# Optimization experiments

Hardware: AMD Instinct MI355X
Metric: run time of the kernel (lower is better)

The kernel has to match this reference:

```python
import jax, jax.numpy as jnp
import numpy as np

B, T, D = 8, 1024, 1024
KD, VD, H = 1024, 1024, 16  # key_dim_total, value_dim_total, num_heads
NEG = -1e9
EPS = 1e-5


def setup_inputs() -> dict:
    key = jax.random.key(0)
    ks = jax.random.split(key, 8)
    x = jax.random.normal(ks[0], (B, T, D), dtype=jnp.float32)
    x_lens = jax.random.randint(ks[1], (B,), 1, T + 1).astype(jnp.int32)
    ln_gamma = jnp.ones((D,), jnp.float32)
    ln_beta = jnp.zeros((D,), jnp.float32)
    qkv_out = 2 * KD + VD
    w_qkv = jax.random.normal(ks[2], (D, qkv_out), jnp.float32) / np.sqrt(D)
    b_qkv = jax.random.normal(ks[3], (qkv_out,), jnp.float32) * 0.01
    w_out = jax.random.normal(ks[4], (VD, D), jnp.float32) / np.sqrt(VD)
    b_out = jax.random.normal(ks[5], (D,), jnp.float32) * 0.01
    return {"x": x, "x_lens": x_lens, "ln_gamma": ln_gamma, "ln_beta": ln_beta,
            "w_qkv": w_qkv, "b_qkv": b_qkv, "w_out": w_out, "b_out": b_out}


def reference(x, x_lens, ln_gamma, ln_beta, w_qkv, b_qkv, w_out, b_out):
    # LayerNorm over feature dim
    mu = jnp.mean(x, axis=-1, keepdims=True)
    var = jnp.mean(jnp.square(x - mu), axis=-1, keepdims=True)
    xn = (x - mu) * jax.lax.rsqrt(var + EPS) * ln_gamma + ln_beta
    # fused QKV projection
    qkv = xn @ w_qkv + b_qkv  # (B, T, 2*KD+VD)
    q, k, v = qkv[..., :KD], qkv[..., KD:2 * KD], qkv[..., 2 * KD:]
    hd = KD // H
    q = q.reshape(B, T, H, hd).transpose(0, 2, 1, 3)  # (B,H,T,hd)
    k = k.reshape(B, T, H, hd).transpose(0, 2, 1, 3)
    v = v.reshape(B, T, H, VD // H).transpose(0, 2, 1, 3)
    scale = 1.0 / np.sqrt(hd)
    scores = jnp.einsum("bhtd,bhsd->bhts", q, k) * scale  # (B,H,T,T)
    # combined causal + kv-length padding mask (additive in original; boolean here)
    causal = jnp.tril(jnp.ones((T, T), bool))  # (T,T)
    kv_valid = jnp.arange(T)[None, :] < x_lens[:, None]  # (B,T)
    mask = causal[None, None, :, :] & kv_valid[:, None, None, :]
    scores = jnp.where(mask, scores, NEG)
    att = jax.nn.softmax(scores, axis=-1)
    att_out = jnp.einsum("bhts,bhsd->bhtd", att, v)  # (B,H,T,hd_v)
    out = att_out.transpose(0, 2, 1, 3).reshape(B, T, VD)
    out = out @ w_out + b_out
    return out
```

## Files before the change

kernel.cpp:

```cpp
#include <hip/hip_runtime.h>

#define D_MODEL 1024
#define T_SEQ   1024
#define BATCH   8
#define NHEAD   16
#define HDIM    64

typedef float      v4f   __attribute__((ext_vector_type(4)));
typedef _Float16   half8 __attribute__((ext_vector_type(8)));
typedef _Float16   half4h __attribute__((ext_vector_type(4)));
typedef unsigned int ui4 __attribute__((ext_vector_type(4)));

__device__ __forceinline__ void load_lds16(const _Float16* g, _Float16* l) {
  __builtin_amdgcn_global_load_lds(
      (const __attribute__((address_space(1))) unsigned int*)g,
      (__attribute__((address_space(3))) unsigned int*)l, 16, 0, 0);
}

__global__ __launch_bounds__(256) void ln_kernel(const float* __restrict__ x,
                                                 const float* __restrict__ gamma,
                                                 const float* __restrict__ beta,
                                                 _Float16* __restrict__ xn) {
  int row = blockIdx.x;
  int tid = threadIdx.x;
  const float* xr = x + (size_t)row * D_MODEL;
  v4f xv = *(const v4f*)(xr + tid * 4);
  float s  = xv[0] + xv[1] + xv[2] + xv[3];
  float sq = xv[0]*xv[0] + xv[1]*xv[1] + xv[2]*xv[2] + xv[3]*xv[3];
#pragma unroll
  for (int off = 32; off > 0; off >>= 1) {
    s  += __shfl_xor(s, off);
    sq += __shfl_xor(sq, off);
  }
  __shared__ float ps[4], psq[4];
  int wave = tid >> 6;
  if ((tid & 63) == 0) { ps[wave] = s; psq[wave] = sq; }
  __syncthreads();
  float tot  = ps[0] + ps[1] + ps[2] + ps[3];
  float totq = psq[0] + psq[1] + psq[2] + psq[3];
  float mean = tot * (1.0f / D_MODEL);
  float var  = totq * (1.0f / D_MODEL) - mean * mean;
  float rs   = rsqrtf(var + 1e-5f);
  v4f gv = *(const v4f*)(gamma + tid * 4);
  v4f bv = *(const v4f*)(beta + tid * 4);
  half4h o;
#pragma unroll
  for (int i = 0; i < 4; ++i)
    o[i] = (_Float16)((xv[i] - mean) * rs * gv[i] + bv[i]);
  *(half4h*)(xn + (size_t)row * D_MODEL + tid * 4) = o;
}

__global__ __launch_bounds__(256) void fragize_kernel(const float* __restrict__ W,
                                                      _Float16* __restrict__ Bf,
                                                      int N, int K) {
  int g = blockIdx.x * 256 + threadIdx.x;
  int lane = g & 63, tile = g >> 6;
  int ktiles = K >> 5;
  int kt = tile % ktiles, nt = tile / ktiles;
  int n  = nt * 16 + (lane & 15);
  int k0 = kt * 32 + (lane >> 4) * 8;
  half8 o;
#pragma unroll
  for (int j = 0; j < 8; ++j) o[j] = (_Float16)W[(size_t)(k0 + j) * N + n];
  *(half8*)(Bf + (size_t)g * 8) = o;
}

__global__ __launch_bounds__(256) void wtrans_kernel(const float* __restrict__ W,
                                                     _Float16* __restrict__ Wt,
                                                     int N, int K) {
  __shared__ _Float16 t[64][72];
  int k0 = blockIdx.x * 64, n0 = blockIdx.y * 64;
  int tid = threadIdx.x;
  int r = tid >> 3, c = (tid & 7) * 8;
#pragma unroll
  for (int it = 0; it < 2; ++it) {
    int row = r + it * 32;
    const float* src = W + (size_t)(k0 + row) * N + n0 + c;
    v4f x0 = *(const v4f*)src;
    v4f x1 = *(const v4f*)(src + 4);
#pragma unroll
    for (int j = 0; j < 4; ++j) t[row][c + j] = (_Float16)x0[j];
#pragma unroll
    for (int j = 0; j < 4; ++j) t[row][c + 4 + j] = (_Float16)x1[j];
  }
  __syncthreads();
#pragma unroll
  for (int it = 0; it < 2; ++it) {
    int d = r + it * 32;
    half8 o;
#pragma unroll
    for (int j = 0; j < 8; ++j) o[j] = t[c + j][d];
    *(half8*)(Wt + (size_t)(n0 + d) * K + k0 + c) = o;
  }
}

__global__ __launch_bounds__(256) void vtrans_kernel(const _Float16* __restrict__ Vd,
                                                     _Float16* __restrict__ Vt) {
  __shared__ _Float16 tile[64][68];
  int p  = blockIdx.y;
  int t0 = blockIdx.x * 64;
  int tid = threadIdx.x;
  int r = tid >> 3, c = (tid & 7) * 8;
#pragma unroll
  for (int it = 0; it < 2; ++it) {
    int rr = r + it * 32;
    *(ui4*)&tile[rr][c] = *(const ui4*)&Vd[((size_t)p * T_SEQ + t0 + rr) * HDIM + c];
  }
  __syncthreads();
#pragma unroll
  for (int it = 0; it < 2; ++it) {
    int d = r + it * 32;
    half8 o;
#pragma unroll
    for (int j = 0; j < 8; ++j) o[j] = tile[c + j][d];
    *(half8*)&Vt[((size_t)p * HDIM + d) * T_SEQ + t0 + c] = o;
  }
}


#define BAR   __builtin_amdgcn_s_barrier()
#define LGKM0 asm volatile("s_waitcnt lgkmcnt(0)" ::: "memory")
#define VMC2  asm volatile("s_waitcnt vmcnt(2)" ::: "memory")
#define PRIO1 __builtin_amdgcn_s_setprio(1)
#define PRIO0 __builtin_amdgcn_s_setprio(0)

#define RDA(dst, BUF, KK)                                                       \
  _Pragma("unroll")                                                             \
  for (int d2 = 0; d2 < 4; ++d2)                                                \
    dst[d2] = *(const half8*)(lds + (BUF) +                                     \
                              (wm + d2 * 16 + l15) * 64 +                       \
                              ((((KK) * 4 + quad) ^ swz) * 8));

#define RDB(dst, BUF, NI0, KK)                                                  \
  _Pragma("unroll")                                                             \
  for (int n2 = 0; n2 < 2; ++n2)                                                \
    dst[n2] = *(const half8*)(lds + (BUF) + 8192 +                              \
                              (wn + ((NI0) + n2) * 16 + l15) * 64 +             \
                              ((((KK) * 4 + quad) ^ swz) * 8));

#define MFQ(A_, B_, NI0)                                                        \
  _Pragma("unroll")                                                             \
  for (int mi = 0; mi < 4; ++mi)                                                \
    _Pragma("unroll")                                                           \
    for (int n2 = 0; n2 < 2; ++n2)                                              \
      acc[mi][(NI0) + n2] = __builtin_amdgcn_mfma_f32_16x16x32_f16(             \
          A_[mi], B_[n2], acc[mi][(NI0) + n2], 0, 0, 0);

#define STGA(BUF, R0, KT)                                                       \
  load_lds16(Asrc + (size_t)(R0) * 1024 + (KT) * 64, ldst + (BUF) + (R0) * 64)
#define STGB(BUF, R0, KT)                                                       \
  load_lds16(Bsrc + (size_t)(R0) * 1024 + (KT) * 64, ldst + (BUF) + 8192 + (R0) * 64)

__global__ __launch_bounds__(512, 2) void gemm256_qkv(
    const _Float16* __restrict__ A, const _Float16* __restrict__ Bt,
    const float* __restrict__ bias,
    _Float16* __restrict__ Qd, _Float16* __restrict__ Kd, _Float16* __restrict__ Vd) {
  __shared__ _Float16 lds[49152];
  const int K = 1024;
  int tid  = threadIdx.x;
  int wave = tid >> 6, lane = tid & 63;
  int l15  = lane & 15, quad = lane >> 4;
  int wm = (wave & 1) * 64, wn = (wave >> 1) * 64;
  int m0 = blockIdx.x * 128, n0 = blockIdx.y * 256;
  int swz = l15 & 7;

  int ric = tid >> 3;
  int colofs = ((tid & 7) ^ (ric & 7)) * 8;
  const _Float16* Asrc = A  + (size_t)(m0 + ric) * K + colofs;
  const _Float16* Bsrc = Bt + (size_t)(n0 + ric) * K + colofs;
  _Float16* ldst = lds + wave * 512;

  const int B0 = 0, B1 = 24576;
  v4f acc[4][4];
  v4f zero = {0.f, 0.f, 0.f, 0.f};
#pragma unroll
  for (int i = 0; i < 4; ++i)
#pragma unroll
    for (int j = 0; j < 4; ++j) acc[i][j] = zero;

  STGA(B0, 0, 0); STGA(B0, 64, 0);
  STGB(B0, 0, 0); STGB(B0, 64, 0); STGB(B0, 128, 0); STGB(B0, 192, 0);
  STGA(B1, 0, 1); STGA(B1, 64, 1);
  VMC2; BAR;

  half8 a0[4], a1[4], bl[2], bh[2];
#pragma unroll 1
  for (int i = 0; i < 8; ++i) {
    int kt1 = 2 * i + 1;
    int kt2 = (2 * i + 2 < 16) ? 2 * i + 2 : 15;
    int kt3 = (2 * i + 3 < 16) ? 2 * i + 3 : 15;
    RDA(a0, B0, 0); RDB(bl, B0, 0, 0);
    STGB(B1, 0, kt1); STGB(B1, 64, kt1);
    BAR; LGKM0; PRIO1; MFQ(a0, bl, 0); PRIO0; BAR;
    RDB(bh, B0, 2, 0);
    STGB(B1, 128, kt1); STGB(B1, 192, kt1);
    BAR; LGKM0; PRIO1; MFQ(a0, bh, 2); PRIO0; BAR;
    RDA(a1, B0, 1); RDB(bl, B0, 0, 1);
    BAR; LGKM0; PRIO1; MFQ(a1, bl, 0); PRIO0; BAR;
    RDB(bh, B0, 2, 1);
    STGA(B0, 0, kt2); STGA(B0, 64, kt2);
    VMC2; BAR; LGKM0; PRIO1; MFQ(a1, bh, 2); PRIO0; BAR;
    RDA(a0, B1, 0); RDB(bl, B1, 0, 0);
    STGB(B0, 0, kt2); STGB(B0, 64, kt2);
    BAR; LGKM0; PRIO1; MFQ(a0, bl, 0); PRIO0; BAR;
    RDB(bh, B1, 2, 0);
    STGB(B0, 128, kt2); STGB(B0, 192, kt2);
    BAR; LGKM0; PRIO1; MFQ(a0, bh, 2); PRIO0; BAR;
    RDA(a1, B1, 1); RDB(bl, B1, 0, 1);
    BAR; LGKM0; PRIO1; MFQ(a1, bl, 0); PRIO0; BAR;
    RDB(bh, B1, 2, 1);
    STGA(B1, 0, kt3); STGA(B1, 64, kt3);
    VMC2; BAR; LGKM0; PRIO1; MFQ(a1, bh, 2); PRIO0; BAR;
  }

  float bv[4];
#pragma unroll
  for (int ni = 0; ni < 4; ++ni) bv[ni] = bias[n0 + wn + ni * 16 + l15];
  int sec = n0 >> 10;
  _Float16* dstP = sec == 0 ? Qd : (sec == 1 ? Kd : Vd);
  float scale = sec == 0 ? 0.18033688f : 1.0f;
#pragma unroll
  for (int mi = 0; mi < 4; ++mi)
#pragma unroll
    for (int ni = 0; ni < 4; ++ni) {
      int n = n0 + wn + ni * 16 + l15;
      int h = (n >> 6) & 15, d = n & 63;
#pragma unroll
      for (int r = 0; r < 4; ++r) {
        int m = m0 + wm + mi * 16 + quad * 4 + r;
        int b = m >> 10, t = m & 1023;
        float v = acc[mi][ni][r] + bv[ni];
        dstP[((size_t)(b * NHEAD + h) * T_SEQ + t) * HDIM + d] = (_Float16)(v * scale);
      }
    }
}

template <int MODE>
__global__ __launch_bounds__(256) void gemm_kernel(
    const _Float16* __restrict__ A, const _Float16* __restrict__ Bfrag,
    const float* __restrict__ bias, int M, int N, int K,
    float* __restrict__ outF,
    _Float16* __restrict__ Qd, _Float16* __restrict__ Kd, _Float16* __restrict__ Vd) {
  __shared__ _Float16 As[2][128 * 32];
  int tid = threadIdx.x;
  int wave = tid >> 6, lane = tid & 63;
  int l15 = lane & 15, quad = lane >> 4;
  int wm = (wave & 1) * 64, wn = (wave >> 1) * 64;
  int m0 = blockIdx.x * 128, n0 = blockIdx.y * 128;
  v4f zero = {0.f, 0.f, 0.f, 0.f};
  v4f acc[4][4];
#pragma unroll
  for (int i = 0; i < 4; ++i)
#pragma unroll
    for (int j = 0; j < 4; ++j) acc[i][j] = zero;

  int ar0 = tid >> 2;
  int akc = (tid & 3) * 8;
  const _Float16* Ap = A + (size_t)(m0 + ar0) * K + akc;
  _Float16* AsW0 = &As[0][0] + wave * 512;
  _Float16* AsW1 = &As[1][0] + wave * 512;
  const int ktiles = K >> 5;
  const _Float16* Bp = Bfrag + (size_t)((n0 + wn) >> 4) * ktiles * 512 + lane * 8;

  load_lds16(Ap, AsW0);
  load_lds16(Ap + (size_t)64 * K, AsW0 + 2048);
  for (int kt = 0; kt < ktiles; ++kt) {
    int cur = kt & 1;
    __syncthreads();
    if (kt + 1 < ktiles) {
      _Float16* nx = cur ? AsW0 : AsW1;
      load_lds16(Ap + (kt + 1) * 32,                  nx);
      load_lds16(Ap + (kt + 1) * 32 + (size_t)64 * K, nx + 2048);
    }
    half8 bf[4];
#pragma unroll
    for (int ni = 0; ni < 4; ++ni)
      bf[ni] = *(const half8*)(Bp + ((size_t)ni * ktiles + kt) * 512);
    half8 af[4];
#pragma unroll
    for (int i = 0; i < 4; ++i)
      af[i] = *(const half8*)&As[cur][(wm + i * 16 + l15) * 32 + quad * 8];
#pragma unroll
    for (int mi = 0; mi < 4; ++mi)
#pragma unroll
      for (int ni = 0; ni < 4; ++ni)
        acc[mi][ni] = __builtin_amdgcn_mfma_f32_16x16x32_f16(af[mi], bf[ni], acc[mi][ni], 0, 0, 0);
  }
  float bv[4];
#pragma unroll
  for (int ni = 0; ni < 4; ++ni) bv[ni] = bias[n0 + wn + ni * 16 + l15];
#pragma unroll
  for (int mi = 0; mi < 4; ++mi) {
#pragma unroll
    for (int ni = 0; ni < 4; ++ni) {
      int n = n0 + wn + ni * 16 + l15;
#pragma unroll
      for (int r = 0; r < 4; ++r) {
        int m = m0 + wm + mi * 16 + quad * 4 + r;
        float v = acc[mi][ni][r] + bv[ni];
        if (MODE == 1) {
          outF[(size_t)m * N + n] = v;
        } else {
          int b = m >> 10, t = m & 1023;
          int h = (n >> 6) & 15, d = n & 63;
          size_t idx = ((size_t)(b * NHEAD + h) * T_SEQ + t) * HDIM + d;
          if (n < 1024)        Qd[idx] = (_Float16)(v * 0.18033688f);
          else if (n < 2048)   Kd[idx] = (_Float16)v;
          else                 Vd[idx] = (_Float16)v;
        }
      }
    }
  }
}

__global__ __launch_bounds__(256) void attn_kernel(const _Float16* __restrict__ Qg,
                                                   const _Float16* __restrict__ Kk,
                                                   const _Float16* __restrict__ Vt,
                                                   const int* __restrict__ x_lens,
                                                   _Float16* __restrict__ att) {
  __shared__ _Float16 Ks[2][64 * 32];
  __shared__ _Float16 Vs[2][64 * 32];
  __shared__ _Float16 Pb[4][16 * 72];
  int blk = blockIdx.x;
  int qt = blk >> 7;
  int bh = blk & 127;
  int h  = bh & 15;
  int b  = bh >> 4;
  int t0 = qt * 64;
  int len = x_lens[b];
  int tid = threadIdx.x;
  int wave = tid >> 6, lane = tid & 63;
  int l15 = lane & 15, quad = lane >> 4;
  size_t plane = (size_t)(b * NHEAD + h) * (T_SEQ * HDIM);
  int qrow = t0 + wave * 16;
  int qabs = qrow + l15;
  const _Float16* Qp = Qg + plane + (size_t)qabs * HDIM + quad * 8;
  half8 qf0 = *(const half8*)Qp;
  half8 qf1 = *(const half8*)(Qp + 32);
  v4f zero = {0.f, 0.f, 0.f, 0.f};
  float m_i = -1e30f, l_i = 0.f;
  v4f Ov[4];
#pragma unroll
  for (int nt = 0; nt < 4; ++nt) Ov[nt] = zero;

  int jmaxb = min(t0 + 63, len - 1);
  int ntile = (jmaxb >> 6) + 1;
  int wjmax = min(qrow + 15, len - 1);

  const _Float16* src[4];
  _Float16* dst[4];
  int strd[4];
#pragma unroll
  for (int i = 0; i < 4; ++i) {
    int u = wave * 4 + i;
    int q = u & 3, hf = (u >> 2) & 1;
    if (u < 8) {
      src[i] = Kk + plane + (size_t)(q * 16 + (lane >> 2)) * HDIM + hf * 32 + (lane & 3) * 8;
      dst[i] = &Ks[hf][0] + q * 512;
      strd[i] = 64 * HDIM;
    } else {
      src[i] = Vt + plane + (size_t)(q * 16 + (lane >> 2)) * T_SEQ + hf * 32 + (lane & 3) * 8;
      dst[i] = &Vs[hf][0] + q * 512;
      strd[i] = 64;
    }
  }

  for (int jt = 0; jt < ntile; ++jt) {
    int j0 = jt * 64;
    __syncthreads();
#pragma unroll
    for (int i = 0; i < 4; ++i) {
      load_lds16(src[i], dst[i]);
      src[i] += strd[i];
    }
    __syncthreads();
    if (j0 <= wjmax) {
      v4f s[4];
#pragma unroll
      for (int nt = 0; nt < 4; ++nt) {
        s[nt] = zero;
        half8 k0 = *(const half8*)&Ks[0][(nt * 16 + l15) * 32 + quad * 8];
        half8 k1 = *(const half8*)&Ks[1][(nt * 16 + l15) * 32 + quad * 8];
        s[nt] = __builtin_amdgcn_mfma_f32_16x16x32_f16(k0, qf0, s[nt], 0, 0, 0);
        s[nt] = __builtin_amdgcn_mfma_f32_16x16x32_f16(k1, qf1, s[nt], 0, 0, 0);
      }
      float mnew = m_i;
      bool full = (j0 + 63 <= qrow) && (j0 + 63 < len);
      if (full) {
#pragma unroll
        for (int nt = 0; nt < 4; ++nt)
#pragma unroll
          for (int r = 0; r < 4; ++r)
            mnew = fmaxf(mnew, s[nt][r]);
      } else {
#pragma unroll
        for (int nt = 0; nt < 4; ++nt) {
#pragma unroll
          for (int r = 0; r < 4; ++r) {
            int key = j0 + nt * 16 + quad * 4 + r;
            float v = (key <= qabs && key < len) ? s[nt][r] : -1e30f;
            s[nt][r] = v;
            mnew = fmaxf(mnew, v);
          }
        }
      }
      mnew = fmaxf(mnew, __shfl_xor(mnew, 16));
      mnew = fmaxf(mnew, __shfl_xor(mnew, 32));
      float alpha = exp2f(m_i - mnew);
      m_i = mnew;
      float rsum = 0.f;
#pragma unroll
      for (int nt = 0; nt < 4; ++nt)
#pragma unroll
        for (int r = 0; r < 4; ++r) {
          float p = exp2f(s[nt][r] - mnew);
          s[nt][r] = p;
          rsum += p;
        }
      rsum += __shfl_xor(rsum, 16);
      rsum += __shfl_xor(rsum, 32);
      l_i = l_i * alpha + rsum;
#pragma unroll
      for (int nt = 0; nt < 4; ++nt)
#pragma unroll
        for (int r = 0; r < 4; ++r) Ov[nt][r] *= alpha;
#pragma unroll
      for (int nt = 0; nt < 4; ++nt) {
        half4h pk;
#pragma unroll
        for (int r = 0; r < 4; ++r) pk[r] = (_Float16)s[nt][r];
        *(half4h*)&Pb[wave][l15 * 72 + nt * 16 + quad * 4] = pk;
      }
      asm volatile("s_waitcnt lgkmcnt(0)" ::: "memory");
      half8 pf0 = *(const half8*)&Pb[wave][l15 * 72 + quad * 8];
      half8 pf1 = *(const half8*)&Pb[wave][l15 * 72 + 32 + quad * 8];
#pragma unroll
      for (int nt = 0; nt < 4; ++nt) {
        half8 v0 = *(const half8*)&Vs[0][(nt * 16 + l15) * 32 + quad * 8];
        half8 v1 = *(const half8*)&Vs[1][(nt * 16 + l15) * 32 + quad * 8];
        Ov[nt] = __builtin_amdgcn_mfma_f32_16x16x32_f16(v0, pf0, Ov[nt], 0, 0, 0);
        Ov[nt] = __builtin_amdgcn_mfma_f32_16x16x32_f16(v1, pf1, Ov[nt], 0, 0, 0);
      }
    }
  }
  float inv = 1.0f / l_i;
#pragma unroll
  for (int nt = 0; nt < 4; ++nt) {
    half4h ok;
#pragma unroll
    for (int r = 0; r < 4; ++r) ok[r] = (_Float16)(Ov[nt][r] * inv);
    *(half4h*)&Pb[wave][l15 * 72 + nt * 16 + quad * 4] = ok;
  }
  asm volatile("s_waitcnt lgkmcnt(0)" ::: "memory");
  int r0 = lane >> 3, c0 = (lane & 7) * 8;
  half8 o0 = *(const half8*)&Pb[wave][r0 * 72 + c0];
  half8 o1 = *(const half8*)&Pb[wave][(r0 + 8) * 72 + c0];
  *(half8*)&att[((size_t)(b * T_SEQ) + qrow + r0) * D_MODEL + h * HDIM + c0] = o0;
  *(half8*)&att[((size_t)(b * T_SEQ) + qrow + r0 + 8) * D_MODEL + h * HDIM + c0] = o1;
}

extern "C" void kernel_launch(void* const* d_in, const int* in_sizes, int n_in,
                              void* d_out, int out_size, void* d_ws, size_t ws_size,
                              hipStream_t stream) {
  const float* x        = (const float*)d_in[0];
  const int*   x_lens   = (const int*)d_in[1];
  const float* ln_gamma = (const float*)d_in[2];
  const float* ln_beta  = (const float*)d_in[3];
  const float* w_qkv    = (const float*)d_in[4];
  const float* b_qkv    = (const float*)d_in[5];
  const float* w_out    = (const float*)d_in[6];
  const float* b_out    = (const float*)d_in[7];
  float* out = (float*)d_out;

  char* w = (char*)d_ws;
  _Float16* xn    = (_Float16*)w; w += (size_t)8192 * 1024 * 2;
  _Float16* WtQKV = (_Float16*)w; w += (size_t)3072 * 1024 * 2;
  _Float16* BfOut = (_Float16*)w; w += (size_t)1024 * 1024 * 2;
  _Float16* Qd    = (_Float16*)w; w += (size_t)8192 * 1024 * 2;
  _Float16* Kd    = (_Float16*)w; w += (size_t)8192 * 1024 * 2;
  _Float16* Vd    = (_Float16*)w; w += (size_t)8192 * 1024 * 2;
  _Float16* att   = (_Float16*)w; w += (size_t)8192 * 1024 * 2;
  _Float16* Vt    = xn;

  wtrans_kernel<<<dim3(16, 48), 256, 0, stream>>>(w_qkv, WtQKV, 3072, 1024);
  fragize_kernel<<<(1024 * 1024 / 8) / 256, 256, 0, stream>>>(w_out, BfOut, 1024, 1024);
  ln_kernel<<<8192, 256, 0, stream>>>(x, ln_gamma, ln_beta, xn);
  gemm256_qkv<<<dim3(64, 12), 512, 0, stream>>>(xn, WtQKV, b_qkv, Qd, Kd, Vd);
  vtrans_kernel<<<dim3(16, 128), 256, 0, stream>>>(Vd, Vt);
  attn_kernel<<<2048, 256, 0, stream>>>(Qd, Kd, Vt, x_lens, att);
  gemm_kernel<1><<<dim3(8192 / 128, 1024 / 128), 256, 0, stream>>>(
      att, BfOut, b_out, 8192, 1024, 1024, out, nullptr, nullptr, nullptr);
}
```

Baseline: 246.0 us.

## Enlarge QKV GEMM block tile to 256x256 with restaged pipeline

Doubles the M tile of the QKV projection GEMM from 128 to 256 rows per block, so each wave computes a 128x64 sub-tile with 8x4 accumulators. The LDS double buffers grow to 128 KB total, and the A/B staging and MFMA schedule are reordered so each B fragment is reused across two A halves. The goal is higher arithmetic intensity and less global/LDS traffic per FLOP. In exchange it raises register pressure and LDS usage, may drop occupancy below the requested 2 blocks per CU, and halves the grid to 384 blocks on 256 CUs, which risks tail imbalance.

```diff
diff --git a/kernel.cpp b/kernel.cpp
--- a/kernel.cpp
+++ b/kernel.cpp
@@ -124,44 +124,47 @@
 #define PRIO1 __builtin_amdgcn_s_setprio(1)
 #define PRIO0 __builtin_amdgcn_s_setprio(0)
 
-#define RDA(dst, BUF, KK)                                                       \
+#define RDA(dst, BUF, MI0, KK)                                                  \
   _Pragma("unroll")                                                             \
   for (int d2 = 0; d2 < 4; ++d2)                                                \
     dst[d2] = *(const half8*)(lds + (BUF) +                                     \
-                              (wm + d2 * 16 + l15) * 64 +                       \
+                              (wm + ((MI0) + d2) * 16 + l15) * 64 +             \
                               ((((KK) * 4 + quad) ^ swz) * 8));
 
-#define RDB(dst, BUF, NI0, KK)                                                  \
+#define RDB(dst, BUF, KK)                                                       \
   _Pragma("unroll")                                                             \
-  for (int n2 = 0; n2 < 2; ++n2)                                                \
-    dst[n2] = *(const half8*)(lds + (BUF) + 8192 +                              \
-                              (wn + ((NI0) + n2) * 16 + l15) * 64 +             \
+  for (int ni = 0; ni < 4; ++ni)                                                \
+    dst[ni] = *(const half8*)(lds + (BUF) + 16384 +                             \
+                              (wn + ni * 16 + l15) * 64 +                       \
                               ((((KK) * 4 + quad) ^ swz) * 8));
 
-#define MFQ(A_, B_, NI0)                                                        \
+#define MFQ(MI0, A_, B_)                                                        \
   _Pragma("unroll")                                                             \
   for (int mi = 0; mi < 4; ++mi)                                                \
     _Pragma("unroll")                                                           \
-    for (int n2 = 0; n2 < 2; ++n2)                                              \
-      acc[mi][(NI0) + n2] = __builtin_amdgcn_mfma_f32_16x16x32_f16(             \
-          A_[mi], B_[n2], acc[mi][(NI0) + n2], 0, 0, 0);
+    for (int ni = 0; ni < 4; ++ni)                                              \
+      acc[(MI0) + mi][ni] = __builtin_amdgcn_mfma_f32_16x16x32_f16(             \
+          A_[mi], B_[ni], acc[(MI0) + mi][ni], 0, 0, 0);
 
 #define STGA(BUF, R0, KT)                                                       \
   load_lds16(Asrc + (size_t)(R0) * 1024 + (KT) * 64, ldst + (BUF) + (R0) * 64)
 #define STGB(BUF, R0, KT)                                                       \
-  load_lds16(Bsrc + (size_t)(R0) * 1024 + (KT) * 64, ldst + (BUF) + 8192 + (R0) * 64)
+  load_lds16(Bsrc + (size_t)(R0) * 1024 + (KT) * 64, ldst + (BUF) + 16384 + (R0) * 64)
+#define HTA(BUF, HH, KT) { STGA(BUF, (HH)*128, KT); STGA(BUF, (HH)*128 + 64, KT); }
+#define HTB(BUF, KT)     { STGB(BUF, 0, KT);   STGB(BUF, 64, KT);                 \
+                           STGB(BUF, 128, KT); STGB(BUF, 192, KT); }
 
 __global__ __launch_bounds__(512, 2) void gemm256_qkv(
     const _Float16* __restrict__ A, const _Float16* __restrict__ Bt,
     const float* __restrict__ bias,
     _Float16* __restrict__ Qd, _Float16* __restrict__ Kd, _Float16* __restrict__ Vd) {
-  __shared__ _Float16 lds[49152];
+  __shared__ _Float16 lds[65536];
   const int K = 1024;
   int tid  = threadIdx.x;
   int wave = tid >> 6, lane = tid & 63;
   int l15  = lane & 15, quad = lane >> 4;
-  int wm = (wave & 1) * 64, wn = (wave >> 1) * 64;
-  int m0 = blockIdx.x * 128, n0 = blockIdx.y * 256;
+  int wm = (wave & 1) * 128, wn = (wave >> 1) * 64;
+  int m0 = blockIdx.x * 256, n0 = blockIdx.y * 256;
   int swz = l15 & 7;
 
   int ric = tid >> 3;
@@ -170,47 +173,44 @@
   const _Float16* Bsrc = Bt + (size_t)(n0 + ric) * K + colofs;
   _Float16* ldst = lds + wave * 512;
 
-  const int B0 = 0, B1 = 24576;
-  v4f acc[4][4];
+  const int B0 = 0, B1 = 32768;
+  v4f acc[8][4];
   v4f zero = {0.f, 0.f, 0.f, 0.f};
 #pragma unroll
-  for (int i = 0; i < 4; ++i)
+  for (int i = 0; i < 8; ++i)
 #pragma unroll
     for (int j = 0; j < 4; ++j) acc[i][j] = zero;
 
-  STGA(B0, 0, 0); STGA(B0, 64, 0);
-  STGB(B0, 0, 0); STGB(B0, 64, 0); STGB(B0, 128, 0); STGB(B0, 192, 0);
-  STGA(B1, 0, 1); STGA(B1, 64, 1);
+  HTA(B0, 0, 0); HTA(B0, 1, 0); HTB(B0, 0);
+  HTA(B1, 0, 1);
   VMC2; BAR;
 
-  half8 a0[4], a1[4], bl[2], bh[2];
+  half8 a0[4], a1[4], b0[4], b1[4];
 #pragma unroll 1
   for (int i = 0; i < 8; ++i) {
     int kt1 = 2 * i + 1;
     int kt2 = (2 * i + 2 < 16) ? 2 * i + 2 : 15;
     int kt3 = (2 * i + 3 < 16) ? 2 * i + 3 : 15;
-    RDA(a0, B0, 0); RDB(bl, B0, 0, 0);
-    STGB(B1, 0, kt1); STGB(B1, 64, kt1);
-    BAR; LGKM0; PRIO1; MFQ(a0, bl, 0); PRIO0; BAR;
-    RDB(bh, B0, 2, 0);
-    STGB(B1, 128, kt1); STGB(B1, 192, kt1);
-    BAR; LGKM0; PRIO1; MFQ(a0, bh, 2); PRIO0; BAR;
-    RDA(a1, B0, 1); RDB(bl, B0, 0, 1);
-    BAR; LGKM0; PRIO1; MFQ(a1, bl, 0); PRIO0; BAR;
-    RDB(bh, B0, 2, 1);
-    STGA(B0, 0, kt2); STGA(B0, 64, kt2);
-    VMC2; BAR; LGKM0; PRIO1; MFQ(a1, bh, 2); PRIO0; BAR;
-    RDA(a0, B1, 0); RDB(bl, B1, 0, 0);
-    STGB(B0, 0, kt2); STGB(B0, 64, kt2);
-    BAR; LGKM0; PRIO1; MFQ(a0, bl, 0); PRIO0; BAR;
-    RDB(bh, B1, 2, 0);
-    STGB(B0, 128, kt2); STGB(B0, 192, kt2);
-    BAR; LGKM0; PRIO1; MFQ(a0, bh, 2); PRIO0; BAR;
-    RDA(a1, B1, 1); RDB(bl, B1, 0, 1);
-    BAR; LGKM0; PRIO1; MFQ(a1, bl, 0); PRIO0; BAR;
-    RDB(bh, B1, 2, 1);
-    STGA(B1, 0, kt3); STGA(B1, 64, kt3);
-    VMC2; BAR; LGKM0; PRIO1; MFQ(a1, bh, 2); PRIO0; BAR;
+    RDA(a0, B0, 0, 0); RDB(b0, B0, 0);
+    HTA(B1, 1, kt1);
+    BAR; LGKM0; PRIO1; MFQ(0, a0, b0); PRIO0; BAR;
+    RDA(a1, B0, 4, 0);
+    HTB(B1, kt1);
+    BAR; LGKM0; PRIO1; MFQ(4, a1, b0); PRIO0; BAR;
+    RDA(a0, B0, 0, 1); RDA(a1, B0, 4, 1); RDB(b1, B0, 1);
+    BAR; LGKM0; PRIO1; MFQ(0, a0, b1); PRIO0; BAR;
+    HTA(B0, 0, kt2);
+    VMC2; BAR; PRIO1; MFQ(4, a1, b1); PRIO0; BAR;
+    RDA(a0, B1, 0, 0); RDB(b0, B1, 0);
+    HTA(B0, 1, kt2);
+    BAR; LGKM0; PRIO1; MFQ(0, a0, b0); PRIO0; BAR;
+    RDA(a1, B1, 4, 0);
+    HTB(B0, kt2);
+    BAR; LGKM0; PRIO1; MFQ(4, a1, b0); PRIO0; BAR;
+    RDA(a0, B1, 0, 1); RDA(a1, B1, 4, 1); RDB(b1, B1, 1);
+    BAR; LGKM0; PRIO1; MFQ(0, a0, b1); PRIO0; BAR;
+    HTA(B1, 0, kt3);
+    VMC2; BAR; PRIO1; MFQ(4, a1, b1); PRIO0; BAR;
   }
 
   float bv[4];
@@ -220,7 +220,7 @@
   _Float16* dstP = sec == 0 ? Qd : (sec == 1 ? Kd : Vd);
   float scale = sec == 0 ? 0.18033688f : 1.0f;
 #pragma unroll
-  for (int mi = 0; mi < 4; ++mi)
+  for (int mi = 0; mi < 8; ++mi)
 #pragma unroll
     for (int ni = 0; ni < 4; ++ni) {
       int n = n0 + wn + ni * 16 + l15;
@@ -485,7 +485,7 @@
   wtrans_kernel<<<dim3(16, 48), 256, 0, stream>>>(w_qkv, WtQKV, 3072, 1024);
   fragize_kernel<<<(1024 * 1024 / 8) / 256, 256, 0, stream>>>(w_out, BfOut, 1024, 1024);
   ln_kernel<<<8192, 256, 0, stream>>>(x, ln_gamma, ln_beta, xn);
-  gemm256_qkv<<<dim3(64, 12), 512, 0, stream>>>(xn, WtQKV, b_qkv, Qd, Kd, Vd);
+  gemm256_qkv<<<dim3(32, 12), 512, 0, stream>>>(xn, WtQKV, b_qkv, Qd, Kd, Vd);
   vtrans_kernel<<<dim3(16, 128), 256, 0, stream>>>(Vd, Vt);
   attn_kernel<<<2048, 256, 0, stream>>>(Qd, Kd, Vt, x_lens, att);
   gemm_kernel<1><<<dim3(8192 / 128, 1024 / 128), 256, 0, stream>>>(
```

Result: slower. 254.7 us (+3.6%).
